# Kernel tuning notes

Hardware: AMD Instinct MI355X
Metric: run time of the kernel (lower is better)

The kernel has to match this reference:

```python
import jax, jax.numpy as jnp
import numpy as np

N_NODES = 100000
N_EDGES = 1600000
K_IND = 16          # num_indicator_weight (distance bins)
K_MLP = 16          # num_mlp_weight
DIM_HIDDEN = 64     # dim_mlp_hidden
DIST_MAX = 1.0      # distance_max
K = K_IND + K_MLP   # node feature dim / Dense output dim


def setup_inputs() -> dict:
    key = jax.random.key(0)
    ks = jax.random.split(key, 10)
    nodes = jax.random.normal(ks[0], (N_NODES, K), dtype=jnp.float32)
    distance = jax.random.uniform(ks[1], (N_EDGES,), dtype=jnp.float32) * DIST_MAX
    receivers = jnp.sort(jax.random.randint(ks[2], (N_EDGES,), 0, N_NODES, dtype=jnp.int32))
    senders = jax.random.randint(ks[3], (N_EDGES,), 0, N_NODES, dtype=jnp.int32)
    edges_padding = jnp.ones((N_EDGES,), dtype=jnp.float32)
    # MLPWeights params (Dense(1->H), Dense(H->K_MLP))
    w1 = jax.random.normal(ks[4], (1, DIM_HIDDEN), dtype=jnp.float32) / np.sqrt(1.0)
    b1 = jnp.zeros((DIM_HIDDEN,), dtype=jnp.float32)
    w2 = jax.random.normal(ks[5], (DIM_HIDDEN, K_MLP), dtype=jnp.float32) / np.sqrt(DIM_HIDDEN)
    b2 = jnp.zeros((K_MLP,), dtype=jnp.float32)
    # PowerDifference params (a=0.5, b=2)
    a = jnp.array([0.5], dtype=jnp.float32)
    b = jnp.array([2.0], dtype=jnp.float32)
    # gamma_self (no bias), gamma_gathered (with bias), both Dense(K->K)
    wg_self = jax.random.normal(ks[6], (K, K), dtype=jnp.float32) / np.sqrt(K)
    wg_gath = jax.random.normal(ks[7], (K, K), dtype=jnp.float32) / np.sqrt(K)
    bg_gath = jnp.zeros((K,), dtype=jnp.float32)
    return {"nodes": nodes, "distance": distance, "edges_padding": edges_padding,
            "receivers": receivers, "senders": senders,
            "w1": w1, "b1": b1, "w2": w2, "b2": b2,
            "a": a, "b": b, "wg_self": wg_self, "wg_gath": wg_gath, "bg_gath": bg_gath}


def _normalize_edges(edges, seg_ids, num_segments):
    sums = jax.ops.segment_sum(edges, seg_ids, num_segments=num_segments, indices_are_sorted=True)
    return edges / (sums[seg_ids] + 1e-5)


def _softmax_edges(edges, seg_ids, num_segments):
    maxs = jax.ops.segment_max(edges, seg_ids, num_segments=num_segments, indices_are_sorted=True)
    e = jnp.exp(edges - maxs[seg_ids])
    sums = jax.ops.segment_sum(e, seg_ids, num_segments=num_segments, indices_are_sorted=True)
    return e / sums[seg_ids]


def reference(nodes, distance, edges_padding, receivers, senders,
              w1, b1, w2, b2, a, b, wg_self, wg_gath, bg_gath):
    n = nodes.shape[0]
    d = distance[:, None]                                   # [E,1]
    # IndicatorWeights: bin membership via heaviside of product
    bins = jnp.linspace(0.0, DIST_MAX, K_IND + 1, dtype=nodes.dtype)
    indicator = jnp.heaviside((bins[None, :-1] - d) * (d - bins[None, 1:]), 0.0)  # [E,K_IND]
    indicator_w = _normalize_edges(indicator, receivers, n)
    # MLPWeights: Dense -> relu -> Dense, then segment softmax
    mlp = jax.nn.relu(d @ w1 + b1) @ w2 + b2                # [E,K_MLP]
    mlp_w = _softmax_edges(mlp, receivers, n)
    weights = jnp.concatenate([indicator_w, mlp_w], axis=1) * edges_padding[:, None]  # [E,K]
    # PowerDifference on gathered node pairs
    a_c = jnp.clip(a, 0.0, 1.0)
    b_c = jnp.abs(b)
    edge_pds = jnp.power(jnp.abs(a_c * nodes[receivers] - (1.0 - a_c) * nodes[senders]), b_c)  # [E,K]
    gathered = jax.ops.segment_sum(weights * edge_pds, receivers, num_segments=n, indices_are_sorted=True)  # [N,K]
    out = jax.nn.relu(nodes @ wg_self + (gathered @ wg_gath + bg_gath))
    return out
```

## Files before the change

### kernel.cpp

```cpp
#include <hip/hip_runtime.h>
#include <math.h>

#define K_TOT 32
#define K_IND 16
#define K_MLP 16
#define DHID  64


__global__ void prep_kernel(const int* __restrict__ recv, int E, int N,
                            const float* __restrict__ w1,
                            const float* __restrict__ b1,
                            const float* __restrict__ w2,
                            float* __restrict__ wsP,
                            float* __restrict__ wsN,
                            int* __restrict__ wsflag,
                            int* __restrict__ rp) {
    if (blockIdx.x == 0 && threadIdx.x < 64) {
        int t = threadIdx.x;
        if (t < K_MLP) {
            float P = 0.f, Nn = 0.f;
            for (int j = 0; j < DHID; ++j) {
                float w = w1[j];
                float v = w2[j * K_MLP + t];
                P  += fmaxf(w, 0.f) * v;
                Nn += fminf(w, 0.f) * v;
            }
            wsP[t] = P; wsN[t] = Nn;
        }
        bool nz = (b1[t] != 0.f);
        unsigned long long mask = __ballot(nz);
        if (t == 0) *wsflag = (mask == 0ull) ? 1 : 0;
    }
    int tid = blockIdx.x * blockDim.x + threadIdx.x;
    if (tid <= N) {
        int lo = 0, hi = E;
        while (lo < hi) {
            int mid = (lo + hi) >> 1;
            if (recv[mid] < tid) lo = mid + 1; else hi = mid;
        }
        rp[tid] = lo;
    }
}

__global__ __launch_bounds__(256) void graph_kernel(
        const float* __restrict__ nodes,
        const float* __restrict__ dist,
        const float* __restrict__ padv,
        const int*   __restrict__ send,
        const float* __restrict__ w1,
        const float* __restrict__ b1,
        const float* __restrict__ w2,
        const float* __restrict__ b2,
        const float* __restrict__ a_p,
        const float* __restrict__ b_p,
        const float* __restrict__ wg_self,
        const float* __restrict__ wg_gath,
        const float* __restrict__ bg,
        const float* __restrict__ wsP,
        const float* __restrict__ wsN,
        const int*   __restrict__ wsflag,
        const int*   __restrict__ rp,
        float* __restrict__ out,
        int N) {
    int wave = blockIdx.x * (blockDim.x >> 6) + (threadIdx.x >> 6);
    if (wave >= N) return;
    int n    = wave;
    int lane = threadIdx.x & 63;
    int eg   = lane >> 4;
    int cc   = lane & 15;

    float a_c = fminf(fmaxf(a_p[0], 0.f), 1.f);
    float am  = 1.f - a_c;
    float bc  = fabsf(b_p[0]);

    float Pk = wsP[cc];
    float Nk = wsN[cc];

    const float* nrow = nodes + n * K_TOT;
    float nr0 = nrow[cc];
    float nr1 = nrow[cc + 16];
    float anr0 = a_c * nr0;
    float anr1 = a_c * nr1;

    int e0 = rp[n], eEnd = rp[n + 1];
    int len = eEnd - e0;

    float lo = (float)cc * 0.0625f;
    float hi = lo + 0.0625f;

    float cnt = 0.f, si = 0.f;
    float l = 0.f, acc = 0.f;
    float g_ind, g_mlp;

    bool fastf = (*wsflag != 0) && (bc == 2.0f) && (len <= 64);

    if (__builtin_amdgcn_readfirstlane((int)fastf)) {
        if (len > 0) {
            int idx = lane < len ? lane : len - 1;
            float dm = fabsf(dist[e0 + idx]);
#pragma unroll
            for (int off = 32; off; off >>= 1) dm = fmaxf(dm, __shfl_xor(dm, off));
            float negM = -fmaxf(fabsf(Pk), fabsf(Nk)) * dm;

            int nG = (len + 3) >> 2;
            int last = len - 1;

#define GRP_BODY(G)                                                          \
            {                                                                \
                int i = ((G) << 2) + eg;                                     \
                bool valid = i < len;                                        \
                int ii = valid ? i : last;                                   \
                float d  = dist[e0 + ii];                                    \
                int   s  = send[e0 + ii];                                    \
                float pe = padv[e0 + ii];                                    \
                const float* nsrow = nodes + (s * K_TOT + cc);               \
                float ns0 = nsrow[0];                                        \
                float ns1 = nsrow[16];                                       \
                float t0 = fmaf(-am, ns0, anr0);                             \
                float t1 = fmaf(-am, ns1, anr1);                             \
                float pd0 = t0 * t0;                                         \
                float pd1 = t1 * t1;                                         \
                bool inb = valid && (d > lo) && (d < hi);                    \
                cnt += inb ? 1.f : 0.f;                                      \
                si   = inb ? fmaf(pe, pd0, si) : si;                         \
                float q = (d > 0.f) ? Pk : Nk;                               \
                float p = __expf(fmaf(d, q, negM));                          \
                p = valid ? p : 0.f;                                         \
                l += p;                                                      \
                acc = fmaf(p, pe * pd1, acc);                                \
            }

            int g = 0;
            for (; g + 2 <= nG; g += 2) {
                GRP_BODY(g)
                GRP_BODY(g + 1)
            }
            if (g < nG) {
                GRP_BODY(g)
            }
#undef GRP_BODY
        }

#pragma unroll
        for (int off = 16; off <= 32; off <<= 1) {
            cnt += __shfl_xor(cnt, off);
            si  += __shfl_xor(si,  off);
            l   += __shfl_xor(l,   off);
            acc += __shfl_xor(acc, off);
        }
        g_ind = si / (cnt + 1e-5f);
        g_mlp = (l > 0.f) ? (acc / l) : 0.f;
    } else {
        float m_on = -INFINITY;
        for (int i = eg; i < len; i += 4) {
            int e = e0 + i;
            float d  = dist[e];
            int   s  = send[e];
            float pe = padv[e];
            const float* nsrow = nodes + (s * K_TOT + cc);
            float ns0 = nsrow[0];
            float ns1 = nsrow[16];
            float t0 = fabsf(fmaf(-am, ns0, anr0));
            float t1 = fabsf(fmaf(-am, ns1, anr1));
            float pd0 = powf(t0, bc);
            float pd1 = powf(t1, bc);

            bool inb = (d > lo) && (d < hi);
            cnt += inb ? 1.f : 0.f;
            si  += inb ? pe * pd0 : 0.f;

            float mlp = 0.f;
            for (int j = 0; j < DHID; ++j) {
                float h = fmaxf(fmaf(d, w1[j], b1[j]), 0.f);
                mlp = fmaf(h, w2[j * K_MLP + cc], mlp);
            }
            float mn = fmaxf(m_on, mlp);
            float al = (m_on == -INFINITY) ? 0.f : __expf(m_on - mn);
            float p  = __expf(mlp - mn);
            l   = fmaf(l, al, p);
            acc = fmaf(acc, al, p * pe * pd1);
            m_on = mn;
        }
#pragma unroll
        for (int off = 16; off <= 32; off <<= 1) {
            cnt += __shfl_xor(cnt, off);
            si  += __shfl_xor(si,  off);
            float m2 = __shfl_xor(m_on, off), l2 = __shfl_xor(l, off), a2 = __shfl_xor(acc, off);
            float mn = fmaxf(m_on, m2);
            float f1 = (m_on == -INFINITY) ? 0.f : __expf(m_on - mn);
            float f2 = (m2   == -INFINITY) ? 0.f : __expf(m2 - mn);
            l   = l * f1 + l2 * f2;
            acc = acc * f1 + a2 * f2;
            m_on = mn;
        }
        g_ind = si / (cnt + 1e-5f);
        g_mlp = (l > 0.f) ? (acc / l) : 0.f;
    }

    int h  = lane >> 5;
    int oc = lane & 31;
    float pre_g = ((lane >> 4) & 1) ? g_mlp : g_ind;
    float pre_n = ((lane >> 4) & 1) ? nr1 : nr0;

    float o_s = 0.f, o_g = 0.f;
    int jbase = h * 16;
#pragma unroll
    for (int jj = 0; jj < 16; ++jj) {
        int j = jbase + jj;
        float gj = __shfl(pre_g, j);
        float nj = __shfl(pre_n, j);
        o_s = fmaf(nj, wg_self[j * K_TOT + oc], o_s);
        o_g = fmaf(gj, wg_gath[j * K_TOT + oc], o_g);
    }
    float o = o_s + o_g;
    o += __shfl_xor(o, 32);
    if (h == 0) {
        out[n * K_TOT + oc] = fmaxf(o + bg[oc], 0.f);
    }
}

extern "C" void kernel_launch(void* const* d_in, const int* in_sizes, int n_in,
                              void* d_out, int out_size, void* d_ws, size_t ws_size,
                              hipStream_t stream) {
    const float* nodes   = (const float*)d_in[0];
    const float* dist    = (const float*)d_in[1];
    const float* padv    = (const float*)d_in[2];
    const int*   recv    = (const int*)d_in[3];
    const int*   send    = (const int*)d_in[4];
    const float* w1      = (const float*)d_in[5];
    const float* b1      = (const float*)d_in[6];
    const float* w2      = (const float*)d_in[7];
    const float* b2      = (const float*)d_in[8];
    const float* a_p     = (const float*)d_in[9];
    const float* b_p     = (const float*)d_in[10];
    const float* wg_self = (const float*)d_in[11];
    const float* wg_gath = (const float*)d_in[12];
    const float* bg      = (const float*)d_in[13];
    float* out = (float*)d_out;

    int N = in_sizes[0] / K_TOT;
    int E = in_sizes[1];

    float* wsf    = (float*)d_ws;
    float* wsP    = wsf;
    float* wsN    = wsf + 16;
    int*   wsflag = (int*)d_ws + 32;
    int*   rp     = (int*)d_ws + 64;

    prep_kernel<<<(N + 1 + 255) / 256, 256, 0, stream>>>(recv, E, N, w1, b1, w2,
                                                         wsP, wsN, wsflag, rp);
    graph_kernel<<<(N + 3) / 4, 256, 0, stream>>>(
        nodes, dist, padv, send, w1, b1, w2, b2, a_p, b_p,
        wg_self, wg_gath, bg, wsP, wsN, wsflag, rp, out, N);
}
```

Before: 172.2 us.

## Split graph kernel into edge-parallel LDS-atomic aggregation and node output kernel

Replaces the one-wave-per-node kernel with an edge-parallel kernel. Each block takes a fixed chunk of 512 edges and accumulates per-receiver partial sums in LDS with atomics. Boundary receivers are merged into a global accumulator with global atomics, or all rows are when a chunk spans too many receivers. A second kernel then normalizes the sums and applies the two dense layers, handling two nodes per wave. The aim is to remove load imbalance and per-node latency, at the cost of a large workspace memset, an extra write and read of a per-node accumulator, extra receiver-row gathers and LDS atomic contention. The old path remains as a fallback when the workspace is too small.

```diff
diff --git a/kernel.cpp b/kernel.cpp
--- a/kernel.cpp
+++ b/kernel.cpp
@@ -5,7 +5,9 @@
 #define K_IND 16
 #define K_MLP 16
 #define DHID  64
-
+#define EB    512
+#define CAP   96
+#define ROWS  68
 
 __global__ void prep_kernel(const int* __restrict__ recv, int E, int N,
                             const float* __restrict__ w1,
@@ -42,7 +44,235 @@
     }
 }
 
-__global__ __launch_bounds__(256) void graph_kernel(
+__global__ __launch_bounds__(256) void edge_kernel(
+        const float* __restrict__ nodes,
+        const float* __restrict__ dist,
+        const float* __restrict__ padv,
+        const int*   __restrict__ send,
+        const int*   __restrict__ recv,
+        const float* __restrict__ a_p,
+        const float* __restrict__ b_p,
+        const float* __restrict__ wsP,
+        const float* __restrict__ wsN,
+        const int*   __restrict__ wsflag,
+        float* __restrict__ gacc,
+        int E) {
+    bool fastf = (*wsflag != 0) && (fabsf(b_p[0]) == 2.0f);
+    if (!fastf) return;
+
+    __shared__ float lds[CAP * ROWS];
+    int tid = threadIdx.x;
+    int e0 = blockIdx.x * EB;
+    int eEnd = e0 + EB; if (eEnd > E) eEnd = E;
+
+    for (int i = tid; i < (CAP * ROWS) / 4; i += 256)
+        ((float4*)lds)[i] = make_float4(0.f, 0.f, 0.f, 0.f);
+
+    int rFirst = recv[e0];
+    int rLast  = recv[eEnd - 1];
+    int span = rLast - rFirst + 1;
+    bool overflow = span > CAP;
+    __syncthreads();
+
+    int lane = tid & 63;
+    int wid  = tid >> 6;
+    int esub = lane >> 4;
+    int cc   = lane & 15;
+
+    float a_c = fminf(fmaxf(a_p[0], 0.f), 1.f);
+    float am  = 1.f - a_c;
+    float Pk  = wsP[cc];
+    float Nk  = wsN[cc];
+    float negM = -fmaxf(fabsf(Pk), fabsf(Nk));
+    float lo = (float)cc * 0.0625f;
+    float hi = lo + 0.0625f;
+
+    int wbeg = e0 + wid * 128;
+    int wend = wbeg + 128; if (wend > eEnd) wend = eEnd;
+
+    if (!overflow) {
+        for (int e = wbeg + esub; e < wend; e += 4) {
+            float d  = dist[e];
+            int   s  = send[e];
+            float pe = padv[e];
+            int   r  = recv[e];
+            float* row = lds + (r - rFirst) * ROWS;
+            const float* nsr = nodes + (s * K_TOT + cc);
+            float ns0 = nsr[0], ns1 = nsr[16];
+            const float* nrr = nodes + (r * K_TOT + cc);
+            float nr0 = nrr[0], nr1 = nrr[16];
+            float t0 = fmaf(a_c, nr0, -(am * ns0));
+            float t1 = fmaf(a_c, nr1, -(am * ns1));
+            float pd0 = t0 * t0, pd1 = t1 * t1;
+            if ((d > lo) && (d < hi)) {
+                atomicAdd(row + cc, 1.f);
+                atomicAdd(row + cc + 16, pe * pd0);
+            }
+            float q = (d > 0.f) ? Pk : Nk;
+            float p = __expf(fmaf(d, q, negM));
+            atomicAdd(row + cc + 32, p);
+            atomicAdd(row + cc + 48, p * (pe * pd1));
+        }
+    } else {
+        for (int e = wbeg + esub; e < wend; e += 4) {
+            float d  = dist[e];
+            int   s  = send[e];
+            float pe = padv[e];
+            int   r  = recv[e];
+            float* row = gacc + (size_t)r * 64;
+            const float* nsr = nodes + (s * K_TOT + cc);
+            float ns0 = nsr[0], ns1 = nsr[16];
+            const float* nrr = nodes + (r * K_TOT + cc);
+            float nr0 = nrr[0], nr1 = nrr[16];
+            float t0 = fmaf(a_c, nr0, -(am * ns0));
+            float t1 = fmaf(a_c, nr1, -(am * ns1));
+            float pd0 = t0 * t0, pd1 = t1 * t1;
+            if ((d > lo) && (d < hi)) {
+                atomicAdd(row + cc, 1.f);
+                atomicAdd(row + cc + 16, pe * pd0);
+            }
+            float q = (d > 0.f) ? Pk : Nk;
+            float p = __expf(fmaf(d, q, negM));
+            atomicAdd(row + cc + 32, p);
+            atomicAdd(row + cc + 48, p * (pe * pd1));
+        }
+    }
+    __syncthreads();
+
+    if (!overflow) {
+        int total = span * 64;
+        for (int i = tid; i < total; i += 256) {
+            int rl = i >> 6;
+            int slot = i & 63;
+            float v = lds[rl * ROWS + slot];
+            int r = rFirst + rl;
+            float* dst = gacc + (size_t)r * 64 + slot;
+            if (r == rFirst || r == rLast) atomicAdd(dst, v);
+            else *dst = v;
+        }
+    }
+}
+
+__global__ __launch_bounds__(256) void node_kernel(
+        const float* __restrict__ nodes,
+        const float* __restrict__ gacc,
+        const float* __restrict__ wg_self,
+        const float* __restrict__ wg_gath,
+        const float* __restrict__ bg,
+        float* __restrict__ out,
+        int N,
+        const float* __restrict__ dist,
+        const float* __restrict__ padv,
+        const int*   __restrict__ send,
+        const int*   __restrict__ rp,
+        const float* __restrict__ w1,
+        const float* __restrict__ b1,
+        const float* __restrict__ w2,
+        const float* __restrict__ a_p,
+        const float* __restrict__ b_p,
+        const int*   __restrict__ wsflag) {
+    int wave = blockIdx.x * 4 + (threadIdx.x >> 6);
+    int lane = threadIdx.x & 63;
+    int n0 = wave * 2;
+    if (n0 >= N) return;
+    int p = lane >> 5;
+    int c = lane & 31;
+    int node = n0 + p;
+    int nld = node < N ? node : N - 1;
+
+    bool fastf = (*wsflag != 0) && (fabsf(b_p[0]) == 2.0f);
+    float pre_g, pre_n;
+
+    if (__builtin_amdgcn_readfirstlane((int)fastf)) {
+        const float* row = gacc + (size_t)nld * 64;
+        int s1 = (c < 16) ? c : c + 16;
+        float v1 = row[s1];
+        float v2 = row[s1 + 16];
+        pre_g = (c < 16) ? v2 / (v1 + 1e-5f)
+                         : ((v1 > 0.f) ? v2 / v1 : 0.f);
+        pre_n = nodes[nld * K_TOT + c];
+    } else {
+        float a_c = fminf(fmaxf(a_p[0], 0.f), 1.f);
+        float am  = 1.f - a_c;
+        float bc  = fabsf(b_p[0]);
+        int eg = lane >> 4, cc = lane & 15;
+        float lo = (float)cc * 0.0625f;
+        float hi = lo + 0.0625f;
+        float gi0 = 0.f, gm0 = 0.f, gi1 = 0.f, gm1 = 0.f;
+        for (int t = 0; t < 2; ++t) {
+            int nn = n0 + t;
+            float g_ind = 0.f, g_mlp = 0.f;
+            if (nn < N) {
+                const float* nrow = nodes + nn * K_TOT;
+                float nr0 = nrow[cc], nr1 = nrow[cc + 16];
+                float anr0 = a_c * nr0, anr1 = a_c * nr1;
+                int e0 = rp[nn], eEnd = rp[nn + 1];
+                float cnt = 0.f, si = 0.f, l = 0.f, acc = 0.f, m_on = -INFINITY;
+                for (int i = e0 + eg; i < eEnd; i += 4) {
+                    float d  = dist[i];
+                    int   s  = send[i];
+                    float pe = padv[i];
+                    const float* nsr = nodes + (s * K_TOT + cc);
+                    float ns0 = nsr[0], ns1 = nsr[16];
+                    float t0 = fabsf(fmaf(-am, ns0, anr0));
+                    float t1 = fabsf(fmaf(-am, ns1, anr1));
+                    float pd0 = powf(t0, bc);
+                    float pd1 = powf(t1, bc);
+                    bool inb = (d > lo) && (d < hi);
+                    cnt += inb ? 1.f : 0.f;
+                    si  += inb ? pe * pd0 : 0.f;
+                    float mlp = 0.f;
+                    for (int j = 0; j < DHID; ++j) {
+                        float h = fmaxf(fmaf(d, w1[j], b1[j]), 0.f);
+                        mlp = fmaf(h, w2[j * K_MLP + cc], mlp);
+                    }
+                    float mn = fmaxf(m_on, mlp);
+                    float al = (m_on == -INFINITY) ? 0.f : __expf(m_on - mn);
+                    float pp = __expf(mlp - mn);
+                    l   = fmaf(l, al, pp);
+                    acc = fmaf(acc, al, pp * pe * pd1);
+                    m_on = mn;
+                }
+#pragma unroll
+                for (int off = 16; off <= 32; off <<= 1) {
+                    cnt += __shfl_xor(cnt, off);
+                    si  += __shfl_xor(si,  off);
+                    float m2 = __shfl_xor(m_on, off), l2 = __shfl_xor(l, off), a2 = __shfl_xor(acc, off);
+                    float mn = fmaxf(m_on, m2);
+                    float f1 = (m_on == -INFINITY) ? 0.f : __expf(m_on - mn);
+                    float f2 = (m2   == -INFINITY) ? 0.f : __expf(m2 - mn);
+                    l   = l * f1 + l2 * f2;
+                    acc = acc * f1 + a2 * f2;
+                    m_on = mn;
+                }
+                g_ind = si / (cnt + 1e-5f);
+                g_mlp = (l > 0.f) ? (acc / l) : 0.f;
+            }
+            if (t == 0) { gi0 = g_ind; gm0 = g_mlp; }
+            else        { gi1 = g_ind; gm1 = g_mlp; }
+        }
+        int srcl = c & 15;
+        float si0 = __shfl(gi0, srcl), si1 = __shfl(gi1, srcl);
+        float sm0 = __shfl(gm0, srcl), sm1 = __shfl(gm1, srcl);
+        float sgi = p ? si1 : si0;
+        float sgm = p ? sm1 : sm0;
+        pre_g = (c < 16) ? sgi : sgm;
+        pre_n = nodes[nld * K_TOT + c];
+    }
+
+    float o = 0.f;
+    int sbase = p << 5;
+#pragma unroll
+    for (int j = 0; j < 32; ++j) {
+        float gj = __shfl(pre_g, sbase + j);
+        float nj = __shfl(pre_n, sbase + j);
+        o = fmaf(nj, wg_self[j * K_TOT + c], o);
+        o = fmaf(gj, wg_gath[j * K_TOT + c], o);
+    }
+    if (node < N) out[node * K_TOT + c] = fmaxf(o + bg[c], 0.f);
+}
+
+__global__ __launch_bounds__(256) void graph_kernel_fb(
         const float* __restrict__ nodes,
         const float* __restrict__ dist,
         const float* __restrict__ padv,
@@ -50,7 +280,6 @@
         const float* __restrict__ w1,
         const float* __restrict__ b1,
         const float* __restrict__ w2,
-        const float* __restrict__ b2,
         const float* __restrict__ a_p,
         const float* __restrict__ b_p,
         const float* __restrict__ wg_self,
@@ -72,26 +301,18 @@
     float a_c = fminf(fmaxf(a_p[0], 0.f), 1.f);
     float am  = 1.f - a_c;
     float bc  = fabsf(b_p[0]);
-
     float Pk = wsP[cc];
     float Nk = wsN[cc];
-
     const float* nrow = nodes + n * K_TOT;
     float nr0 = nrow[cc];
     float nr1 = nrow[cc + 16];
-    float anr0 = a_c * nr0;
-    float anr1 = a_c * nr1;
-
+    float anr0 = a_c * nr0, anr1 = a_c * nr1;
     int e0 = rp[n], eEnd = rp[n + 1];
     int len = eEnd - e0;
-
     float lo = (float)cc * 0.0625f;
     float hi = lo + 0.0625f;
-
-    float cnt = 0.f, si = 0.f;
-    float l = 0.f, acc = 0.f;
+    float cnt = 0.f, si = 0.f, l = 0.f, acc = 0.f;
     float g_ind, g_mlp;
-
     bool fastf = (*wsflag != 0) && (bc == 2.0f) && (len <= 64);
 
     if (__builtin_amdgcn_readfirstlane((int)fastf)) {
@@ -101,46 +322,30 @@
 #pragma unroll
             for (int off = 32; off; off >>= 1) dm = fmaxf(dm, __shfl_xor(dm, off));
             float negM = -fmaxf(fabsf(Pk), fabsf(Nk)) * dm;
-
             int nG = (len + 3) >> 2;
             int last = len - 1;
-
-#define GRP_BODY(G)                                                          \
-            {                                                                \
-                int i = ((G) << 2) + eg;                                     \
-                bool valid = i < len;                                        \
-                int ii = valid ? i : last;                                   \
-                float d  = dist[e0 + ii];                                    \
-                int   s  = send[e0 + ii];                                    \
-                float pe = padv[e0 + ii];                                    \
-                const float* nsrow = nodes + (s * K_TOT + cc);               \
-                float ns0 = nsrow[0];                                        \
-                float ns1 = nsrow[16];                                       \
-                float t0 = fmaf(-am, ns0, anr0);                             \
-                float t1 = fmaf(-am, ns1, anr1);                             \
-                float pd0 = t0 * t0;                                         \
-                float pd1 = t1 * t1;                                         \
-                bool inb = valid && (d > lo) && (d < hi);                    \
-                cnt += inb ? 1.f : 0.f;                                      \
-                si   = inb ? fmaf(pe, pd0, si) : si;                         \
-                float q = (d > 0.f) ? Pk : Nk;                               \
-                float p = __expf(fmaf(d, q, negM));                          \
-                p = valid ? p : 0.f;                                         \
-                l += p;                                                      \
-                acc = fmaf(p, pe * pd1, acc);                                \
-            }
-
-            int g = 0;
-            for (; g + 2 <= nG; g += 2) {
-                GRP_BODY(g)
-                GRP_BODY(g + 1)
-            }
-            if (g < nG) {
-                GRP_BODY(g)
-            }
-#undef GRP_BODY
-        }
-
+            for (int g = 0; g < nG; ++g) {
+                int i = (g << 2) + eg;
+                bool valid = i < len;
+                int ii = valid ? i : last;
+                float d  = dist[e0 + ii];
+                int   s  = send[e0 + ii];
+                float pe = padv[e0 + ii];
+                const float* nsr = nodes + (s * K_TOT + cc);
+                float ns0 = nsr[0], ns1 = nsr[16];
+                float t0 = fmaf(-am, ns0, anr0);
+                float t1 = fmaf(-am, ns1, anr1);
+                float pd0 = t0 * t0, pd1 = t1 * t1;
+                bool inb = valid && (d > lo) && (d < hi);
+                cnt += inb ? 1.f : 0.f;
+                si   = inb ? fmaf(pe, pd0, si) : si;
+                float q = (d > 0.f) ? Pk : Nk;
+                float pp = __expf(fmaf(d, q, negM));
+                pp = valid ? pp : 0.f;
+                l += pp;
+                acc = fmaf(pp, pe * pd1, acc);
+            }
+        }
 #pragma unroll
         for (int off = 16; off <= 32; off <<= 1) {
             cnt += __shfl_xor(cnt, off);
@@ -157,18 +362,14 @@
             float d  = dist[e];
             int   s  = send[e];
             float pe = padv[e];
-            const float* nsrow = nodes + (s * K_TOT + cc);
-            float ns0 = nsrow[0];
-            float ns1 = nsrow[16];
+            const float* nsr = nodes + (s * K_TOT + cc);
+            float ns0 = nsr[0], ns1 = nsr[16];
             float t0 = fabsf(fmaf(-am, ns0, anr0));
             float t1 = fabsf(fmaf(-am, ns1, anr1));
-            float pd0 = powf(t0, bc);
-            float pd1 = powf(t1, bc);
-
+            float pd0 = powf(t0, bc), pd1 = powf(t1, bc);
             bool inb = (d > lo) && (d < hi);
             cnt += inb ? 1.f : 0.f;
             si  += inb ? pe * pd0 : 0.f;
-
             float mlp = 0.f;
             for (int j = 0; j < DHID; ++j) {
                 float h = fmaxf(fmaf(d, w1[j], b1[j]), 0.f);
@@ -176,9 +377,9 @@
             }
             float mn = fmaxf(m_on, mlp);
             float al = (m_on == -INFINITY) ? 0.f : __expf(m_on - mn);
-            float p  = __expf(mlp - mn);
-            l   = fmaf(l, al, p);
-            acc = fmaf(acc, al, p * pe * pd1);
+            float pp = __expf(mlp - mn);
+            l   = fmaf(l, al, pp);
+            acc = fmaf(acc, al, pp * pe * pd1);
             m_on = mn;
         }
 #pragma unroll
@@ -201,7 +402,6 @@
     int oc = lane & 31;
     float pre_g = ((lane >> 4) & 1) ? g_mlp : g_ind;
     float pre_n = ((lane >> 4) & 1) ? nr1 : nr0;
-
     float o_s = 0.f, o_g = 0.f;
     int jbase = h * 16;
 #pragma unroll
@@ -230,7 +430,6 @@
     const float* w1      = (const float*)d_in[5];
     const float* b1      = (const float*)d_in[6];
     const float* w2      = (const float*)d_in[7];
-    const float* b2      = (const float*)d_in[8];
     const float* a_p     = (const float*)d_in[9];
     const float* b_p     = (const float*)d_in[10];
     const float* wg_self = (const float*)d_in[11];
@@ -241,15 +440,37 @@
     int N = in_sizes[0] / K_TOT;
     int E = in_sizes[1];
 
-    float* wsf    = (float*)d_ws;
-    float* wsP    = wsf;
-    float* wsN    = wsf + 16;
-    int*   wsflag = (int*)d_ws + 32;
-    int*   rp     = (int*)d_ws + 64;
-
-    prep_kernel<<<(N + 1 + 255) / 256, 256, 0, stream>>>(recv, E, N, w1, b1, w2,
-                                                         wsP, wsN, wsflag, rp);
-    graph_kernel<<<(N + 3) / 4, 256, 0, stream>>>(
-        nodes, dist, padv, send, w1, b1, w2, b2, a_p, b_p,
-        wg_self, wg_gath, bg, wsP, wsN, wsflag, rp, out, N);
+    size_t gacc_elems = (size_t)N * 64;
+    size_t need = (gacc_elems + 64 + (size_t)N + 1 + 64) * sizeof(float);
+
+    if (ws_size >= need) {
+        float* gacc   = (float*)d_ws;
+        float* meta   = gacc + gacc_elems;
+        float* wsP    = meta;
+        float* wsN    = meta + 16;
+        int*   wsflag = (int*)(meta + 32);
+        int*   rp     = (int*)(meta + 64);
+
+        prep_kernel<<<(N + 1 + 255) / 256, 256, 0, stream>>>(
+            recv, E, N, w1, b1, w2, wsP, wsN, wsflag, rp);
+        hipMemsetAsync(gacc, 0, gacc_elems * sizeof(float), stream);
+        edge_kernel<<<(E + EB - 1) / EB, 256, 0, stream>>>(
+            nodes, dist, padv, send, recv, a_p, b_p, wsP, wsN, wsflag, gacc, E);
+        int nwaves = (N + 1) / 2;
+        node_kernel<<<(nwaves + 3) / 4, 256, 0, stream>>>(
+            nodes, gacc, wg_self, wg_gath, bg, out, N,
+            dist, padv, send, rp, w1, b1, w2, a_p, b_p, wsflag);
+    } else {
+        float* wsf    = (float*)d_ws;
+        float* wsP    = wsf;
+        float* wsN    = wsf + 16;
+        int*   wsflag = (int*)d_ws + 32;
+        int*   rp     = (int*)d_ws + 64;
+
+        prep_kernel<<<(N + 1 + 255) / 256, 256, 0, stream>>>(
+            recv, E, N, w1, b1, w2, wsP, wsN, wsflag, rp);
+        graph_kernel_fb<<<(N + 3) / 4, 256, 0, stream>>>(
+            nodes, dist, padv, send, w1, b1, w2, a_p, b_p,
+            wg_self, wg_gath, bg, wsP, wsN, wsflag, rp, out, N);
+    }
 }
```

Result: slower. 438.8 us (+154.8%).
